# Performance work log

Hardware: AMD Instinct MI355X
Metric: run time of the kernel (lower is better)

The kernel has to match this reference:

```python
import jax, jax.numpy as jnp
import numpy as np

KSIZE = 7      # gaussian kernel size (SecondMomentMatrixLayer default)
SIGMA = 5.0    # gaussian sigma (default)
ALPHA = 0.05   # corner response alpha (CornerResponseLayer default)


def _gaussian_kernel(ksize, sigma):
    ax = np.arange(ksize, dtype=np.float64) - ksize // 2
    g1 = np.exp(-(ax ** 2) / (2.0 * sigma ** 2))
    k2 = np.outer(g1, g1)
    return (k2 / k2.sum()).astype(np.float32)


def setup_inputs() -> dict:
    key = jax.random.key(0)
    x = jax.random.normal(key, (4, 1, 2048, 2048), dtype=jnp.float32)
    # Sobel filters (ImageGradientsLayer): out-channels [Ix, Iy], shape (2,1,3,3)
    sobel_kernel = jnp.array(
        [[[[-1.0, 0.0, 1.0], [-2.0, 0.0, 2.0], [-1.0, 0.0, 1.0]]],
         [[[-1.0, -2.0, -1.0], [0.0, 0.0, 0.0], [1.0, 2.0, 1.0]]]],
        dtype=jnp.float32)
    # Depthwise (groups=3) gaussian kernel, shape (3,1,7,7)
    g = jnp.asarray(_gaussian_kernel(KSIZE, SIGMA))
    gauss_kernel = jnp.tile(g[None, None], (3, 1, 1, 1))
    return {"x": x, "sobel_kernel": sobel_kernel, "gauss_kernel": gauss_kernel}


def _conv(x, k, pad, groups=1):
    # torch Conv2d is cross-correlation; so is lax.conv_general_dilated
    return jax.lax.conv_general_dilated(
        x, k, window_strides=(1, 1), padding=[(pad, pad), (pad, pad)],
        dimension_numbers=("NCHW", "OIHW", "NCHW"), feature_group_count=groups)


def reference(x, sobel_kernel, gauss_kernel):
    # 1) image gradients via Sobel: (N,1,H,W) -> (N,2,H,W)
    grads = _conv(x, sobel_kernel, pad=1)
    Ix, Iy = grads[:, 0], grads[:, 1]
    # 2) channel products: I_xx, I_yy, I_xy -> (N,3,H,W)
    prods = jnp.stack([Ix * Ix, Iy * Iy, Ix * Iy], axis=1)
    # 3) gaussian-weighted second moments (depthwise conv, groups=3)
    S = _conv(prods, gauss_kernel, pad=KSIZE // 2, groups=3)
    Sxx, Syy, Sxy = S[:, 0], S[:, 1], S[:, 2]
    # 4) corner response R = det - alpha * trace^2 -> (N,1,H,W)
    trace = Sxx + Syy
    R = (Sxx * Syy - Sxy * Sxy - ALPHA * trace * trace)[:, None]
    # 5) NMS: global-median threshold, 7x7 stride-1 maxpool, binarize, scale by R
    median = jnp.quantile(R, 0.5, method="lower")  # torch.median = lower median
    thr = jnp.where(R < median, jnp.float32(0.0), R)
    pooled = jax.lax.reduce_window(
        thr, -jnp.inf, jax.lax.max, window_dimensions=(1, 1, 7, 7),
        window_strides=(1, 1, 1, 1),
        padding=[(0, 0), (0, 0), (3, 3), (3, 3)])
    binarized = jnp.where(thr == pooled, jnp.float32(1.0), jnp.float32(0.0))
    return binarized * R
```

## Files before the change

kernel.cpp:

```cpp
#include <hip/hip_runtime.h>
#include <math.h>

constexpr int IMH = 2048, IMW = 2048, NB = 4;
constexpr int NPIX = NB * IMH * IMW;
constexpr unsigned KSEL = 8388607u;

__device__ __forceinline__ unsigned f2u(float f) {
    unsigned b = __float_as_uint(f);
    return (b & 0x80000000u) ? ~b : (b | 0x80000000u);
}

__device__ __forceinline__ void gauss7(float* a) {
    const double g0 = 0.8352702114112720;
    const double g1 = 0.9231163463866358;
    const double g2 = 0.9801986733067553;
    const double s = 2.0 * (g0 + g1 + g2) + 1.0;
    const double inv = 1.0 / s;
    a[0] = a[6] = (float)(g0 * inv);
    a[1] = a[5] = (float)(g1 * inv);
    a[2] = a[4] = (float)(g2 * inv);
    a[3] = (float)inv;
}

__device__ __forceinline__ float2 fmax2(float2 a, float2 b) {
    return make_float2(fmaxf(a.x, b.x), fmaxf(a.y, b.y));
}

template<bool CHK>
__device__ __forceinline__ void sobel_stage(const float* SX, float4* SIXY4,
                                            int x0, int y0, int tid) {
    for (int i = tid; i < 490; i += 256) {
        int s = i / 70, c = i - s * 70;
        int r0 = 6 * s;
        int nr = (s == 6) ? 2 : 6;
        float xa[8], xm[8], xc[8];
        #pragma unroll
        for (int t = 0; t < 8; ++t) {
            if (t < nr + 2) {
                const float* row = SX + (r0 + t) * 72 + c;
                xa[t] = row[0]; xm[t] = row[1]; xc[t] = row[2];
            }
        }
        #pragma unroll
        for (int t = 0; t < 6; ++t) {
            if (t < nr) {
                int r = r0 + t;
                float x00 = xa[t],     x01 = xm[t],     x02 = xc[t];
                float x10 = xa[t + 1],                  x12 = xc[t + 1];
                float x20 = xa[t + 2], x21 = xm[t + 2], x22 = xc[t + 2];
                float ix = (x02 + 2.0f * x12 + x22) - (x00 + 2.0f * x10 + x20);
                float iy = (x20 + 2.0f * x21 + x22) - (x00 + 2.0f * x01 + x02);
                if (CHK) {
                    int gy = y0 - 3 + r, gx = x0 - 3 + c;
                    if (!((unsigned)gy < (unsigned)IMH && (unsigned)gx < (unsigned)IMW)) {
                        ix = 0.f; iy = 0.f;
                    }
                }
                ((float2*)(SIXY4 + r * 36 + (c >> 1)))[c & 1] = make_float2(ix, iy);
            }
        }
    }
}

__launch_bounds__(256, 3)
__global__ void harris_R(const float* __restrict__ x, float* __restrict__ Rout,
                         unsigned* __restrict__ hist) {
    __shared__ __align__(16) float smem[12768];
    float* SX = smem;
    float2* STH2 = (float2*)smem;
    float* STHx = smem + 4864;
    float4* SIXY4 = (float4*)(smem + 7296);
    unsigned* LH = (unsigned*)(smem + 7296);

    const int tid = threadIdx.x;
    const int tx = tid & 63, ty = tid >> 6;
    const int x0 = blockIdx.x * 64, y0 = blockIdx.y * 32, b = blockIdx.z;
    const float* xb = x + (size_t)b * IMH * IMW;
    const bool interior = (x0 >= 4) && (x0 + 68 <= IMW) && (y0 >= 4) && (y0 + 36 <= IMH);

    if (interior) {
        const float* xp = xb + (size_t)(y0 - 4) * IMW + (x0 - 4);
        for (int i = tid; i < 1440; i += 256) {
            int r = i / 36, c2 = i - r * 36;
            *(float2*)&SX[r * 72 + 2 * c2] = *(const float2*)&xp[(size_t)r * IMW + 2 * c2];
        }
    } else {
        for (int i = tid; i < 2880; i += 256) {
            int r = i / 72, c = i - r * 72;
            int gy = y0 - 4 + r, gx = x0 - 4 + c;
            float v = 0.f;
            if ((unsigned)gy < (unsigned)IMH && (unsigned)gx < (unsigned)IMW)
                v = xb[(size_t)gy * IMW + gx];
            SX[r * 72 + c] = v;
        }
    }
    __syncthreads();

    if (interior) sobel_stage<false>(SX, SIXY4, x0, y0, tid);
    else          sobel_stage<true>(SX, SIXY4, x0, y0, tid);
    __syncthreads();

    float a[7]; gauss7(a);

    for (int i = tid; i < 38 * 32; i += 256) {
        int r = i >> 5, p = i & 31;
        const float4* base = SIXY4 + r * 36 + p;
        float4 q0 = base[0], q1 = base[1], q2 = base[2], q3 = base[3];
        float ix8[8] = {q0.x, q0.z, q1.x, q1.z, q2.x, q2.z, q3.x, q3.z};
        float iy8[8] = {q0.y, q0.w, q1.y, q1.w, q2.y, q2.w, q3.y, q3.w};
        float sxxA = 0.f, syyA = 0.f, sxyA = 0.f;
        float sxxB = 0.f, syyB = 0.f, sxyB = 0.f;
        #pragma unroll
        for (int d = 0; d < 7; ++d) {
            float tA = a[d] * ix8[d];
            sxxA += tA * ix8[d];
            sxyA += tA * iy8[d];
            syyA += (a[d] * iy8[d]) * iy8[d];
            float tB = a[d] * ix8[d + 1];
            sxxB += tB * ix8[d + 1];
            sxyB += tB * iy8[d + 1];
            syyB += (a[d] * iy8[d + 1]) * iy8[d + 1];
        }
        *(float4*)&STH2[r * 64 + 2 * p] = make_float4(sxxA, syyA, sxxB, syyB);
        *(float2*)&STHx[r * 64 + 2 * p] = make_float2(sxyA, sxyB);
    }
    __syncthreads();

    for (int i = tid; i < 4096; i += 256) LH[i] = 0u;

    float axx[8] = {0, 0, 0, 0, 0, 0, 0, 0};
    float ayy[8] = {0, 0, 0, 0, 0, 0, 0, 0};
    float axy[8] = {0, 0, 0, 0, 0, 0, 0, 0};
    #pragma unroll
    for (int t = 0; t < 14; ++t) {
        float2 vv = STH2[(8 * ty + t) * 64 + tx];
        float vx = STHx[(8 * ty + t) * 64 + tx];
        #pragma unroll
        for (int j = 0; j < 8; ++j) {
            int d = t - j;
            if (d >= 0 && d < 7) {
                axx[j] += a[d] * vv.x;
                ayy[j] += a[d] * vv.y;
                axy[j] += a[d] * vx;
            }
        }
    }
    float rv[8];
    float* Rb = Rout + (size_t)b * IMH * IMW + (size_t)y0 * IMW + x0;
    #pragma unroll
    for (int j = 0; j < 8; ++j) {
        float sxx = axx[j], syy = ayy[j], sxy = axy[j];
        float tr = sxx + syy;
        float R = sxx * syy - sxy * sxy - 0.05f * tr * tr;
        rv[j] = R;
        Rb[(size_t)(8 * ty + j) * IMW + tx] = R;
    }
    __syncthreads();

    #pragma unroll
    for (int j = 0; j < 8; ++j) atomicAdd(&LH[f2u(rv[j]) >> 20], 1u);
    __syncthreads();

    const unsigned slot = ((blockIdx.z * gridDim.y + blockIdx.y) * gridDim.x + blockIdx.x) & 7u;
    for (int i = tid; i < 4096; i += 256) {
        unsigned c = LH[i];
        if (c) atomicAdd(&hist[i * 8 + slot], c);
    }
}

__global__ void zero_kernel(unsigned* __restrict__ p, int n, int kidx, unsigned kval) {
    int i = blockIdx.x * blockDim.x + threadIdx.x;
    if (i < n) p[i] = (i == kidx) ? kval : 0u;
}

__global__ void hist2_kernel(const float* __restrict__ R, unsigned* __restrict__ hist,
                             const unsigned* __restrict__ sel) {
    __shared__ unsigned lh[4096];
    for (int i = threadIdx.x; i < 4096; i += 256) lh[i] = 0u;
    __syncthreads();
    const unsigned pref = sel[1];
    const float4* R4 = (const float4*)R;
    const int n4 = NPIX / 4;
    for (int i = blockIdx.x * 256 + threadIdx.x; i < n4; i += gridDim.x * 256) {
        float4 v = R4[i];
        unsigned u;
        u = f2u(v.x); if ((u >> 20) == pref) atomicAdd(&lh[(u >> 8) & 0xFFFu], 1u);
        u = f2u(v.y); if ((u >> 20) == pref) atomicAdd(&lh[(u >> 8) & 0xFFFu], 1u);
        u = f2u(v.z); if ((u >> 20) == pref) atomicAdd(&lh[(u >> 8) & 0xFFFu], 1u);
        u = f2u(v.w); if ((u >> 20) == pref) atomicAdd(&lh[(u >> 8) & 0xFFFu], 1u);
    }
    __syncthreads();
    for (int i = threadIdx.x; i < 4096; i += 256) { unsigned c = lh[i]; if (c) atomicAdd(&hist[i], c); }
}

__global__ void hist3_kernel(const float* __restrict__ R, unsigned* __restrict__ hist,
                             const unsigned* __restrict__ sel) {
    __shared__ unsigned lh[256];
    if (threadIdx.x < 256) lh[threadIdx.x] = 0u;
    __syncthreads();
    const unsigned pref = sel[1];
    const float4* R4 = (const float4*)R;
    const int n4 = NPIX / 4;
    for (int i = blockIdx.x * 256 + threadIdx.x; i < n4; i += gridDim.x * 256) {
        float4 v = R4[i];
        unsigned u;
        u = f2u(v.x); if ((u >> 8) == pref) atomicAdd(&lh[u & 0xFFu], 1u);
        u = f2u(v.y); if ((u >> 8) == pref) atomicAdd(&lh[u & 0xFFu], 1u);
        u = f2u(v.z); if ((u >> 8) == pref) atomicAdd(&lh[u & 0xFFu], 1u);
        u = f2u(v.w); if ((u >> 8) == pref) atomicAdd(&lh[u & 0xFFu], 1u);
    }
    __syncthreads();
    { unsigned c = lh[threadIdx.x]; if (c) atomicAdd(&hist[threadIdx.x], c); }
}

__global__ void select_kernel(const unsigned* __restrict__ hist, unsigned* __restrict__ sel,
                              int bpt, int bits, int final_stage, int slots) {
    __shared__ unsigned part[256];
    __shared__ unsigned grp[16];
    __shared__ int chs;
    __shared__ unsigned runs;
    const int t = threadIdx.x;
    const unsigned krem = sel[0];
    unsigned s = 0;
    for (int i = 0; i < bpt; ++i) {
        unsigned bsum = 0;
        for (int j = 0; j < slots; ++j) bsum += hist[(t * bpt + i) * slots + j];
        s += bsum;
    }
    part[t] = s;
    __syncthreads();
    #pragma unroll
    for (int off = 1; off < 256; off <<= 1) {
        unsigned add = (t >= off) ? part[t - off] : 0u;
        __syncthreads();
        part[t] += add;
        __syncthreads();
    }
    unsigned incl = part[t];
    unsigned excl = incl - s;
    if (excl <= krem && krem < incl) { chs = t; runs = excl; }
    __syncthreads();
    int ch = chs;
    if (t < bpt) {
        unsigned g = 0;
        for (int j = 0; j < slots; ++j) g += hist[(ch * bpt + t) * slots + j];
        grp[t] = g;
    }
    __syncthreads();
    if (t == 0) {
        unsigned r2 = runs; int bsel = ch * bpt;
        for (int j = 0; j < bpt; ++j) {
            unsigned h = grp[j];
            if (r2 + h > krem) { bsel = ch * bpt + j; break; }
            r2 += h;
        }
        sel[0] = krem - r2;
        unsigned pref = (sel[1] << bits) | (unsigned)bsel;
        sel[1] = pref;
        if (final_stage) {
            unsigned fb = (pref & 0x80000000u) ? (pref ^ 0x80000000u) : ~pref;
            ((float*)sel)[2] = __uint_as_float(fb);
        }
    }
}

__launch_bounds__(256, 4)
__global__ void harris_out(const float* __restrict__ R, const unsigned* __restrict__ sel,
                           float* __restrict__ out) {
    __shared__ __align__(16) float smem2[9520];
    float* SR = smem2;
    float2* SM2 = (float2*)(smem2 + 5040);
    const float med = ((const float*)sel)[2];
    const int tid = threadIdx.x;
    const int x0 = blockIdx.x * 64, y0 = blockIdx.y * 64, b = blockIdx.z;
    const float* Rb = R + (size_t)b * IMH * IMW;

    for (int i = tid; i < 70 * 70; i += 256) {
        int r = i / 70, c = i - r * 70;
        int gy = y0 - 3 + r, gx = x0 - 3 + c;
        float v = -INFINITY;
        if ((unsigned)gy < (unsigned)IMH && (unsigned)gx < (unsigned)IMW)
            v = Rb[(size_t)gy * IMW + gx];
        SR[r * 72 + c] = v;
    }
    __syncthreads();

    for (int i = tid; i < 70 * 32; i += 256) {
        int r = i >> 5, p = i & 31;
        const float2* u = (const float2*)(SR + r * 72 + 2 * p);
        float2 u0 = u[0], u1 = u[1], u2 = u[2], u3 = u[3];
        float cv[8] = {u0.x, u0.y, u1.x, u1.y, u2.x, u2.y, u3.x, u3.y};
        float tv[8];
        #pragma unroll
        for (int k = 0; k < 8; ++k) {
            float v = cv[k];
            tv[k] = (v < med) ? ((v == -INFINITY) ? -INFINITY : 0.0f) : v;
        }
        float mid = fmaxf(fmaxf(fmaxf(tv[1], tv[2]), fmaxf(tv[3], tv[4])), fmaxf(tv[5], tv[6]));
        SM2[r * 32 + p] = make_float2(fmaxf(tv[0], mid), fmaxf(tv[7], mid));
    }
    __syncthreads();

    const int p = tid & 31, g = tid >> 5;
    float2 vm[14];
    #pragma unroll
    for (int t = 0; t < 14; ++t) vm[t] = SM2[(8 * g + t) * 32 + p];
    float2 m2[13];
    #pragma unroll
    for (int i = 0; i < 13; ++i) m2[i] = fmax2(vm[i], vm[i + 1]);
    float2 m4[11];
    #pragma unroll
    for (int i = 0; i < 11; ++i) m4[i] = fmax2(m2[i], m2[i + 2]);
    float* ob = out + (size_t)b * IMH * IMW + (size_t)y0 * IMW + x0;
    #pragma unroll
    for (int j = 0; j < 8; ++j) {
        float2 pooled = fmax2(m4[j], m4[j + 3]);
        float vA = SR[(8 * g + j + 3) * 72 + 2 * p + 3];
        float vB = SR[(8 * g + j + 3) * 72 + 2 * p + 4];
        float tA = (vA < med) ? 0.0f : vA;
        float tB = (vB < med) ? 0.0f : vB;
        float2 o = make_float2((tA == pooled.x) ? vA : 0.0f, (tB == pooled.y) ? vB : 0.0f);
        *(float2*)&ob[(size_t)(8 * g + j) * IMW + 2 * p] = o;
    }
}

extern "C" void kernel_launch(void* const* d_in, const int* in_sizes, int n_in,
                              void* d_out, int out_size, void* d_ws, size_t ws_size,
                              hipStream_t stream) {
    const float* x = (const float*)d_in[0];
    float* out = (float*)d_out;

    const size_t needed = (size_t)NPIX * 4 + (32768 + 4096 + 256 + 8) * 4;
    if (ws_size < needed) return;
    float* R = (float*)d_ws;
    unsigned* hbase = (unsigned*)((char*)d_ws + (size_t)NPIX * 4);
    unsigned* h1 = hbase;
    unsigned* h2 = hbase + 32768;
    unsigned* h3 = hbase + 36864;
    unsigned* sel = hbase + 37120;

    zero_kernel<<<(37128 + 255) / 256, 256, 0, stream>>>(hbase, 37128, 37120, KSEL);

    dim3 rgrid(IMW / 64, IMH / 32, NB);
    harris_R<<<rgrid, 256, 0, stream>>>(x, R, h1);

    select_kernel<<<1, 256, 0, stream>>>(h1, sel, 16, 12, 0, 8);
    hist2_kernel<<<2048, 256, 0, stream>>>(R, h2, sel);
    select_kernel<<<1, 256, 0, stream>>>(h2, sel, 16, 12, 0, 1);
    hist3_kernel<<<2048, 256, 0, stream>>>(R, h3, sel);
    select_kernel<<<1, 256, 0, stream>>>(h3, sel, 1, 8, 1, 1);

    dim3 ogrid(IMW / 64, IMH / 64, NB);
    harris_out<<<ogrid, 256, 0, stream>>>(R, sel, out);
}
```

Measured before the change: 320.2 us.

## Double threads per block in Harris kernels and simplify per-thread stencil work

```diff
diff --git a/kernel.cpp b/kernel.cpp
--- a/kernel.cpp
+++ b/kernel.cpp
@@ -26,51 +26,14 @@
     return make_float2(fmaxf(a.x, b.x), fmaxf(a.y, b.y));
 }
 
-template<bool CHK>
-__device__ __forceinline__ void sobel_stage(const float* SX, float4* SIXY4,
-                                            int x0, int y0, int tid) {
-    for (int i = tid; i < 490; i += 256) {
-        int s = i / 70, c = i - s * 70;
-        int r0 = 6 * s;
-        int nr = (s == 6) ? 2 : 6;
-        float xa[8], xm[8], xc[8];
-        #pragma unroll
-        for (int t = 0; t < 8; ++t) {
-            if (t < nr + 2) {
-                const float* row = SX + (r0 + t) * 72 + c;
-                xa[t] = row[0]; xm[t] = row[1]; xc[t] = row[2];
-            }
-        }
-        #pragma unroll
-        for (int t = 0; t < 6; ++t) {
-            if (t < nr) {
-                int r = r0 + t;
-                float x00 = xa[t],     x01 = xm[t],     x02 = xc[t];
-                float x10 = xa[t + 1],                  x12 = xc[t + 1];
-                float x20 = xa[t + 2], x21 = xm[t + 2], x22 = xc[t + 2];
-                float ix = (x02 + 2.0f * x12 + x22) - (x00 + 2.0f * x10 + x20);
-                float iy = (x20 + 2.0f * x21 + x22) - (x00 + 2.0f * x01 + x02);
-                if (CHK) {
-                    int gy = y0 - 3 + r, gx = x0 - 3 + c;
-                    if (!((unsigned)gy < (unsigned)IMH && (unsigned)gx < (unsigned)IMW)) {
-                        ix = 0.f; iy = 0.f;
-                    }
-                }
-                ((float2*)(SIXY4 + r * 36 + (c >> 1)))[c & 1] = make_float2(ix, iy);
-            }
-        }
-    }
-}
-
-__launch_bounds__(256, 3)
+__launch_bounds__(512, 6)
 __global__ void harris_R(const float* __restrict__ x, float* __restrict__ Rout,
                          unsigned* __restrict__ hist) {
     __shared__ __align__(16) float smem[12768];
-    float* SX = smem;
-    float2* STH2 = (float2*)smem;
-    float* STHx = smem + 4864;
-    float4* SIXY4 = (float4*)(smem + 7296);
-    unsigned* LH = (unsigned*)(smem + 7296);
+    float2* SIXY = (float2*)smem;
+    float* SX = smem + 5472;
+    float* STH = smem + 5472;
+    unsigned* LH = (unsigned*)smem;
 
     const int tid = threadIdx.x;
     const int tx = tid & 63, ty = tid >> 6;
@@ -80,12 +43,12 @@
 
     if (interior) {
         const float* xp = xb + (size_t)(y0 - 4) * IMW + (x0 - 4);
-        for (int i = tid; i < 1440; i += 256) {
+        for (int i = tid; i < 1440; i += 512) {
             int r = i / 36, c2 = i - r * 36;
             *(float2*)&SX[r * 72 + 2 * c2] = *(const float2*)&xp[(size_t)r * IMW + 2 * c2];
         }
     } else {
-        for (int i = tid; i < 2880; i += 256) {
+        for (int i = tid; i < 2880; i += 512) {
             int r = i / 72, c = i - r * 72;
             int gy = y0 - 4 + r, gx = x0 - 4 + c;
             float v = 0.f;
@@ -96,73 +59,80 @@
     }
     __syncthreads();
 
-    if (interior) sobel_stage<false>(SX, SIXY4, x0, y0, tid);
-    else          sobel_stage<true>(SX, SIXY4, x0, y0, tid);
+    for (int i = tid; i < 2660; i += 512) {
+        int r = i / 70, c = i - r * 70;
+        const float* p = SX + r * 72 + c;
+        float x00 = p[0], x01 = p[1], x02 = p[2];
+        float x10 = p[72], x12 = p[74];
+        float x20 = p[144], x21 = p[145], x22 = p[146];
+        float ix = (x02 + 2.0f * x12 + x22) - (x00 + 2.0f * x10 + x20);
+        float iy = (x20 + 2.0f * x21 + x22) - (x00 + 2.0f * x01 + x02);
+        if (!interior) {
+            int gy = y0 - 3 + r, gx = x0 - 3 + c;
+            if (!((unsigned)gy < (unsigned)IMH && (unsigned)gx < (unsigned)IMW)) {
+                ix = 0.f; iy = 0.f;
+            }
+        }
+        SIXY[r * 72 + c] = make_float2(ix, iy);
+    }
     __syncthreads();
 
     float a[7]; gauss7(a);
 
-    for (int i = tid; i < 38 * 32; i += 256) {
-        int r = i >> 5, p = i & 31;
-        const float4* base = SIXY4 + r * 36 + p;
-        float4 q0 = base[0], q1 = base[1], q2 = base[2], q3 = base[3];
-        float ix8[8] = {q0.x, q0.z, q1.x, q1.z, q2.x, q2.z, q3.x, q3.z};
-        float iy8[8] = {q0.y, q0.w, q1.y, q1.w, q2.y, q2.w, q3.y, q3.w};
-        float sxxA = 0.f, syyA = 0.f, sxyA = 0.f;
-        float sxxB = 0.f, syyB = 0.f, sxyB = 0.f;
+    for (int i = tid; i < 2432; i += 512) {
+        int r = i >> 6, c = i & 63;
+        const float2* p = SIXY + r * 72 + c;
+        float sxx = 0.f, syy = 0.f, sxy = 0.f;
         #pragma unroll
         for (int d = 0; d < 7; ++d) {
-            float tA = a[d] * ix8[d];
-            sxxA += tA * ix8[d];
-            sxyA += tA * iy8[d];
-            syyA += (a[d] * iy8[d]) * iy8[d];
-            float tB = a[d] * ix8[d + 1];
-            sxxB += tB * ix8[d + 1];
-            sxyB += tB * iy8[d + 1];
-            syyB += (a[d] * iy8[d + 1]) * iy8[d + 1];
-        }
-        *(float4*)&STH2[r * 64 + 2 * p] = make_float4(sxxA, syyA, sxxB, syyB);
-        *(float2*)&STHx[r * 64 + 2 * p] = make_float2(sxyA, sxyB);
-    }
-    __syncthreads();
-
-    for (int i = tid; i < 4096; i += 256) LH[i] = 0u;
-
-    float axx[8] = {0, 0, 0, 0, 0, 0, 0, 0};
-    float ayy[8] = {0, 0, 0, 0, 0, 0, 0, 0};
-    float axy[8] = {0, 0, 0, 0, 0, 0, 0, 0};
-    #pragma unroll
-    for (int t = 0; t < 14; ++t) {
-        float2 vv = STH2[(8 * ty + t) * 64 + tx];
-        float vx = STHx[(8 * ty + t) * 64 + tx];
+            float2 v = p[d];
+            float t = a[d] * v.x;
+            sxx += t * v.x;
+            sxy += t * v.y;
+            syy += (a[d] * v.y) * v.y;
+        }
+        STH[r * 64 + c] = sxx;
+        STH[2432 + r * 64 + c] = syy;
+        STH[4864 + r * 64 + c] = sxy;
+    }
+    __syncthreads();
+
+    for (int i = tid; i < 4096; i += 512) LH[i] = 0u;
+
+    float vxx[10], vyy[10], vxy[10];
+    {
+        const float* base = STH + (4 * ty) * 64 + tx;
         #pragma unroll
-        for (int j = 0; j < 8; ++j) {
-            int d = t - j;
-            if (d >= 0 && d < 7) {
-                axx[j] += a[d] * vv.x;
-                ayy[j] += a[d] * vv.y;
-                axy[j] += a[d] * vx;
-            }
-        }
-    }
-    float rv[8];
+        for (int t = 0; t < 10; ++t) {
+            vxx[t] = base[t * 64];
+            vyy[t] = base[2432 + t * 64];
+            vxy[t] = base[4864 + t * 64];
+        }
+    }
+    float rv[4];
     float* Rb = Rout + (size_t)b * IMH * IMW + (size_t)y0 * IMW + x0;
     #pragma unroll
-    for (int j = 0; j < 8; ++j) {
-        float sxx = axx[j], syy = ayy[j], sxy = axy[j];
+    for (int j = 0; j < 4; ++j) {
+        float sxx = 0.f, syy = 0.f, sxy = 0.f;
+        #pragma unroll
+        for (int d = 0; d < 7; ++d) {
+            sxx += a[d] * vxx[j + d];
+            syy += a[d] * vyy[j + d];
+            sxy += a[d] * vxy[j + d];
+        }
         float tr = sxx + syy;
         float R = sxx * syy - sxy * sxy - 0.05f * tr * tr;
         rv[j] = R;
-        Rb[(size_t)(8 * ty + j) * IMW + tx] = R;
-    }
-    __syncthreads();
-
-    #pragma unroll
-    for (int j = 0; j < 8; ++j) atomicAdd(&LH[f2u(rv[j]) >> 20], 1u);
+        Rb[(size_t)(4 * ty + j) * IMW + tx] = R;
+    }
+    __syncthreads();
+
+    #pragma unroll
+    for (int j = 0; j < 4; ++j) atomicAdd(&LH[f2u(rv[j]) >> 20], 1u);
     __syncthreads();
 
     const unsigned slot = ((blockIdx.z * gridDim.y + blockIdx.y) * gridDim.x + blockIdx.x) & 7u;
-    for (int i = tid; i < 4096; i += 256) {
+    for (int i = tid; i < 4096; i += 512) {
         unsigned c = LH[i];
         if (c) atomicAdd(&hist[i * 8 + slot], c);
     }
@@ -264,7 +234,7 @@
     }
 }
 
-__launch_bounds__(256, 4)
+__launch_bounds__(512, 6)
 __global__ void harris_out(const float* __restrict__ R, const unsigned* __restrict__ sel,
                            float* __restrict__ out) {
     __shared__ __align__(16) float smem2[9520];
@@ -275,7 +245,7 @@
     const int x0 = blockIdx.x * 64, y0 = blockIdx.y * 64, b = blockIdx.z;
     const float* Rb = R + (size_t)b * IMH * IMW;
 
-    for (int i = tid; i < 70 * 70; i += 256) {
+    for (int i = tid; i < 70 * 70; i += 512) {
         int r = i / 70, c = i - r * 70;
         int gy = y0 - 3 + r, gx = x0 - 3 + c;
         float v = -INFINITY;
@@ -285,7 +255,7 @@
     }
     __syncthreads();
 
-    for (int i = tid; i < 70 * 32; i += 256) {
+    for (int i = tid; i < 70 * 32; i += 512) {
         int r = i >> 5, p = i & 31;
         const float2* u = (const float2*)(SR + r * 72 + 2 * p);
         float2 u0 = u[0], u1 = u[1], u2 = u[2], u3 = u[3];
@@ -302,25 +272,25 @@
     __syncthreads();
 
     const int p = tid & 31, g = tid >> 5;
-    float2 vm[14];
-    #pragma unroll
-    for (int t = 0; t < 14; ++t) vm[t] = SM2[(8 * g + t) * 32 + p];
-    float2 m2[13];
-    #pragma unroll
-    for (int i = 0; i < 13; ++i) m2[i] = fmax2(vm[i], vm[i + 1]);
-    float2 m4[11];
-    #pragma unroll
-    for (int i = 0; i < 11; ++i) m4[i] = fmax2(m2[i], m2[i + 2]);
+    float2 vm[10];
+    #pragma unroll
+    for (int t = 0; t < 10; ++t) vm[t] = SM2[(4 * g + t) * 32 + p];
+    float2 m2[9];
+    #pragma unroll
+    for (int i = 0; i < 9; ++i) m2[i] = fmax2(vm[i], vm[i + 1]);
+    float2 m4[7];
+    #pragma unroll
+    for (int i = 0; i < 7; ++i) m4[i] = fmax2(m2[i], m2[i + 2]);
     float* ob = out + (size_t)b * IMH * IMW + (size_t)y0 * IMW + x0;
     #pragma unroll
-    for (int j = 0; j < 8; ++j) {
+    for (int j = 0; j < 4; ++j) {
         float2 pooled = fmax2(m4[j], m4[j + 3]);
-        float vA = SR[(8 * g + j + 3) * 72 + 2 * p + 3];
-        float vB = SR[(8 * g + j + 3) * 72 + 2 * p + 4];
+        float vA = SR[(4 * g + j + 3) * 72 + 2 * p + 3];
+        float vB = SR[(4 * g + j + 3) * 72 + 2 * p + 4];
         float tA = (vA < med) ? 0.0f : vA;
         float tB = (vB < med) ? 0.0f : vB;
         float2 o = make_float2((tA == pooled.x) ? vA : 0.0f, (tB == pooled.y) ? vB : 0.0f);
-        *(float2*)&ob[(size_t)(8 * g + j) * IMW + 2 * p] = o;
+        *(float2*)&ob[(size_t)(4 * g + j) * IMW + 2 * p] = o;
     }
 }
 
@@ -342,7 +312,7 @@
     zero_kernel<<<(37128 + 255) / 256, 256, 0, stream>>>(hbase, 37128, 37120, KSEL);
 
     dim3 rgrid(IMW / 64, IMH / 32, NB);
-    harris_R<<<rgrid, 256, 0, stream>>>(x, R, h1);
+    harris_R<<<rgrid, 512, 0, stream>>>(x, R, h1);
 
     select_kernel<<<1, 256, 0, stream>>>(h1, sel, 16, 12, 0, 8);
     hist2_kernel<<<2048, 256, 0, stream>>>(R, h2, sel);
@@ -351,5 +321,5 @@
     select_kernel<<<1, 256, 0, stream>>>(h3, sel, 1, 8, 1, 1);
 
     dim3 ogrid(IMW / 64, IMH / 64, NB);
-    harris_out<<<ogrid, 256, 0, stream>>>(R, sel, out);
-}
+    harris_out<<<ogrid, 512, 0, stream>>>(R, sel, out);
+}
```

Result: faster. 302.0 us (-5.7%).
